# Kernel tuning notes

Hardware: AMD Instinct MI355X
Metric: run time of the kernel (lower is better)

The kernel has to match this reference:

```python
import jax, jax.numpy as jnp
import numpy as np

# dims
B, T = 2, 256            # batch, seq_len
V, H_CP, R = 512, 2, 2   # vocab, CP horizon, CP rank
E, L, NH, NPOS = 768, 12, 12, 1024  # n_embd, n_layer, n_head, max positions
HD = E // NH             # head dim = 64


def _ln(x, g, b, eps=1e-5):
    m = jnp.mean(x, -1, keepdims=True)
    v = jnp.mean((x - m) ** 2, -1, keepdims=True)
    return (x - m) * jax.lax.rsqrt(v + eps) * g + b


def setup_inputs() -> dict:
    key = jax.random.key(0)
    ks = jax.random.split(key, 10)
    s = 0.02  # GPT2 init std
    n = lambda k, sh: s * jax.random.normal(k, sh, jnp.float32)
    return {
        "input_ids": jax.random.randint(ks[0], (B, T), 0, V, dtype=jnp.int32),
        "wte": n(ks[1], (V, E)),
        "wpe": n(ks[2], (NPOS, E)),
        "ln1_g": jnp.ones((L, E), jnp.float32), "ln1_b": jnp.zeros((L, E), jnp.float32),
        "ln2_g": jnp.ones((L, E), jnp.float32), "ln2_b": jnp.zeros((L, E), jnp.float32),
        "w_qkv": n(ks[3], (L, E, 3 * E)), "b_qkv": jnp.zeros((L, 3 * E), jnp.float32),
        "w_ao": n(ks[4], (L, E, E)), "b_ao": jnp.zeros((L, E), jnp.float32),
        "w_fc": n(ks[5], (L, E, 4 * E)), "b_fc": jnp.zeros((L, 4 * E), jnp.float32),
        "w_mo": n(ks[6], (L, 4 * E, E)), "b_mo": jnp.zeros((L, E), jnp.float32),
        "lnf_g": jnp.ones((E,), jnp.float32), "lnf_b": jnp.zeros((E,), jnp.float32),
        "w_cp": n(ks[7], (E, H_CP * V * R)), "b_cp": jnp.zeros((H_CP * V * R,), jnp.float32),
    }


def reference(input_ids, wte, wpe, ln1_g, ln1_b, ln2_g, ln2_b, w_qkv, b_qkv,
              w_ao, b_ao, w_fc, b_fc, w_mo, b_mo, lnf_g, lnf_b, w_cp, b_cp):
    # --- GPT2 transformer body (eval mode: dropout inactive) ---
    h = wte[input_ids] + wpe[:T]                      # (B,T,E)
    causal = jnp.tril(jnp.ones((T, T), bool))
    inv_sqrt_hd = float(1.0 / np.sqrt(HD))

    def block(h, p):
        l1g, l1b, l2g, l2b, wq, bq, wa, ba, wf, bf, wm, bm = p
        x = _ln(h, l1g, l1b)
        qkv = x @ wq + bq                             # (B,T,3E)
        q, k, v = jnp.split(qkv, 3, axis=-1)
        q = q.reshape(B, T, NH, HD).transpose(0, 2, 1, 3)
        k = k.reshape(B, T, NH, HD).transpose(0, 2, 1, 3)
        v = v.reshape(B, T, NH, HD).transpose(0, 2, 1, 3)
        att = jnp.einsum('bhqd,bhkd->bhqk', q, k) * inv_sqrt_hd
        att = jnp.where(causal, att, jnp.float32(-1e9))
        att = jax.nn.softmax(att, axis=-1)
        o = jnp.einsum('bhqk,bhkd->bhqd', att, v).transpose(0, 2, 1, 3).reshape(B, T, E)
        h = h + o @ wa + ba
        x = _ln(h, l2g, l2b)
        h = h + jax.nn.gelu(x @ wf + bf, approximate=True) @ wm + bm  # gelu_new
        return h, None

    h, _ = jax.lax.scan(block, h, (ln1_g, ln1_b, ln2_g, ln2_b, w_qkv, b_qkv,
                                   w_ao, b_ao, w_fc, b_fc, w_mo, b_mo))
    h = _ln(h, lnf_g, lnf_b)                          # last_hidden_state

    # --- CP joint distribution: sum_r outer(f0_r, f1_r), then positivity(exp) ---
    cp = (h.reshape(B * T, E) @ w_cp + b_cp).reshape(B * T, H_CP, V, R)
    scores = jnp.einsum('nir,njr->nij', cp[:, 0], cp[:, 1])  # (B*T, V, V)
    mjd = jnp.exp(scores).reshape(B, T, V, V)[:, :-H_CP].reshape(-1, V, V)

    # --- windowed targets: targets[b,t,h] = input_ids[b, t+1+h] ---
    off = jnp.arange(T - H_CP)[:, None] + 1 + jnp.arange(H_CP)[None, :]
    tgt = input_ids[:, off].reshape(-1, H_CP)         # (B*(T-H), H)

    # --- entropy loss over unnormalized joint: mean(log Z - log p_target) ---
    n = mjd.shape[0]
    p_t = mjd[jnp.arange(n), tgt[:, 0], tgt[:, 1]]
    Z = mjd.sum((1, 2))
    loss = jnp.mean(jnp.log(Z) - jnp.log(p_t))
    return loss
```

## Files before the change

### kernel.cpp

```cpp
#include <hip/hip_runtime.h>

typedef unsigned short u16;
typedef short short8 __attribute__((ext_vector_type(8)));
typedef float f32x4 __attribute__((ext_vector_type(4)));

constexpr int B_  = 2;
constexpr int T_  = 256;
constexpr int V_  = 512;
constexpr int E_  = 768;
constexpr int L_  = 12;
constexpr int NH_ = 12;
constexpr int HD_ = 64;
constexpr int E3_ = 3 * E_;
constexpr int E4_ = 4 * E_;
constexpr int CPD_ = 2048;
constexpr int NTOK_ = B_ * T_;
constexpr int NVALID_ = B_ * (T_ - 2);
constexpr size_t PS_ = (size_t)NTOK_ * E_;
constexpr size_t QS_ = (size_t)NTOK_ * E3_;
constexpr size_t FS_ = (size_t)NTOK_ * E4_;
constexpr size_t CS_ = (size_t)NTOK_ * CPD_;

__device__ __forceinline__ u16 f2b(float f) {
    union { float f; unsigned int u; } c; c.f = f;
    unsigned int r = (c.u + 0x7FFFu + ((c.u >> 16) & 1u)) >> 16; return (u16)r;
}

__global__ __launch_bounds__(256) void embed_k(const int* __restrict__ ids,
    const float* __restrict__ wte, const float* __restrict__ wpe,
    float* __restrict__ h) {
    int n = blockIdx.x;
    int t = n % T_;
    int tok = ids[n];
    for (int e = threadIdx.x; e < E_; e += 256)
        h[n * E_ + e] = wte[tok * E_ + e] + wpe[t * E_ + e];
}

__global__ __launch_bounds__(256) void ln_res_k(float* __restrict__ h,
    const float* __restrict__ pb, int np,
    const float* __restrict__ g, const float* __restrict__ bta,
    u16* __restrict__ out) {
    int n = blockIdx.x;
    int tid = threadIdx.x;
    size_t off = (size_t)n * E_;
    float v0 = h[off + tid], v1 = h[off + tid + 256], v2 = h[off + tid + 512];
    for (int j = 0; j < np; j++) {
        const float* p = pb + (size_t)j * PS_ + off;
        v0 += p[tid]; v1 += p[tid + 256]; v2 += p[tid + 512];
    }
    if (np) { h[off + tid] = v0; h[off + tid + 256] = v1; h[off + tid + 512] = v2; }
    __shared__ float red[256];
    red[tid] = v0 + v1 + v2;
    __syncthreads();
    for (int o = 128; o > 0; o >>= 1) { if (tid < o) red[tid] += red[tid + o]; __syncthreads(); }
    float mean = red[0] * (1.0f / E_);
    __syncthreads();
    float d0 = v0 - mean, d1 = v1 - mean, d2 = v2 - mean;
    red[tid] = d0 * d0 + d1 * d1 + d2 * d2;
    __syncthreads();
    for (int o = 128; o > 0; o >>= 1) { if (tid < o) red[tid] += red[tid + o]; __syncthreads(); }
    float rstd = rsqrtf(red[0] * (1.0f / E_) + 1e-5f);
    u16* y = out + off;
    y[tid]       = f2b(d0 * rstd * g[tid]       + bta[tid]);
    y[tid + 256] = f2b(d1 * rstd * g[tid + 256] + bta[tid + 256]);
    y[tid + 512] = f2b(d2 * rstd * g[tid + 512] + bta[tid + 512]);
}

__global__ __launch_bounds__(512) void mgemm_k(const u16* __restrict__ A,
    const float* __restrict__ W, const float* __restrict__ bias,
    float* __restrict__ outP, int K, int KC, int N) {
    __shared__ u16 As[128 * 40];
    __shared__ u16 Bs[128 * 40];
    int tid = threadIdx.x, lane = tid & 63, wid = tid >> 6;
    int ln15 = lane & 15, quad = lane >> 4;
    int col0 = blockIdx.x * 128, row0 = blockIdx.y * 128;
    int kz = blockIdx.z, kbase = kz * KC;
    int ar = tid >> 2, ak = (tid & 3) * 8;
    const u16* Ag = A + (size_t)(row0 + ar) * K + kbase + ak;
    u16* Aw = &As[ar * 40 + ak];
    int bc = tid & 127, kg = (tid >> 7) * 8;
    const float* Wg = W + (size_t)(kbase + kg) * N + col0 + bc;
    u16* Bw = &Bs[bc * 40 + kg];
    int wr = (wid & 3) * 32, wc = (wid >> 2) * 64;

    f32x4 acc[2][4];
#pragma unroll
    for (int mt = 0; mt < 2; mt++)
#pragma unroll
        for (int nt = 0; nt < 4; nt++) acc[mt][nt] = (f32x4){0.f, 0.f, 0.f, 0.f};

    uint4 av = *(const uint4*)Ag;
    float w[8];
#pragma unroll
    for (int i = 0; i < 8; i++) w[i] = Wg[(size_t)i * N];

    for (int k0 = 0; k0 < KC; k0 += 32) {
        uint4 avn = av;
        float wn[8];
#pragma unroll
        for (int i = 0; i < 8; i++) wn[i] = w[i];
        if (k0 + 32 < KC) {
            avn = *(const uint4*)(Ag + k0 + 32);
#pragma unroll
            for (int i = 0; i < 8; i++) wn[i] = Wg[(size_t)(k0 + 32 + i) * N];
        }
        uint4 bv;
        asm("v_cvt_pk_bf16_f32 %0, %1, %2" : "=v"(bv.x) : "v"(w[0]), "v"(w[1]));
        asm("v_cvt_pk_bf16_f32 %0, %1, %2" : "=v"(bv.y) : "v"(w[2]), "v"(w[3]));
        asm("v_cvt_pk_bf16_f32 %0, %1, %2" : "=v"(bv.z) : "v"(w[4]), "v"(w[5]));
        asm("v_cvt_pk_bf16_f32 %0, %1, %2" : "=v"(bv.w) : "v"(w[6]), "v"(w[7]));
        __syncthreads();
        *(uint4*)Aw = av;
        *(uint4*)Bw = bv;
        __syncthreads();
        short8 af[2], bf[4];
#pragma unroll
        for (int mt = 0; mt < 2; mt++)
            af[mt] = *(const short8*)&As[(wr + mt * 16 + ln15) * 40 + quad * 8];
#pragma unroll
        for (int nt = 0; nt < 4; nt++)
            bf[nt] = *(const short8*)&Bs[(wc + nt * 16 + ln15) * 40 + quad * 8];
#pragma unroll
        for (int mt = 0; mt < 2; mt++)
#pragma unroll
            for (int nt = 0; nt < 4; nt++)
                acc[mt][nt] = __builtin_amdgcn_mfma_f32_16x16x32_bf16(
                    af[mt], bf[nt], acc[mt][nt], 0, 0, 0);
        av = avn;
#pragma unroll
        for (int i = 0; i < 8; i++) w[i] = wn[i];
    }
    float* dst = outP + (size_t)kz * NTOK_ * N;
#pragma unroll
    for (int mt = 0; mt < 2; mt++) {
#pragma unroll
        for (int nt = 0; nt < 4; nt++) {
            int c = col0 + wc + nt * 16 + ln15;
            float bb = (kz == 0) ? bias[c] : 0.f;
#pragma unroll
            for (int r = 0; r < 4; r++) {
                int rw = row0 + wr + mt * 16 + quad * 4 + r;
                dst[(size_t)rw * N + c] = acc[mt][nt][r] + bb;
            }
        }
    }
}

__global__ __launch_bounds__(256) void gelu_k(const float* __restrict__ p0,
    const float* __restrict__ p1, u16* __restrict__ out) {
    size_t i = ((size_t)blockIdx.x * 256 + threadIdx.x) * 4;
    float4 a = *(const float4*)&p0[i];
    float4 b = *(const float4*)&p1[i];
    float u[4] = {a.x + b.x, a.y + b.y, a.z + b.z, a.w + b.w};
    ushort4 o;
    u16* op = (u16*)&o;
#pragma unroll
    for (int j = 0; j < 4; j++) {
        float uu = u[j];
        float inner = 0.7978845608028654f * (uu + 0.044715f * uu * uu * uu);
        op[j] = f2b(0.5f * uu * (1.0f + tanhf(inner)));
    }
    *(ushort4*)&out[i] = o;
}

constexpr int KSTR_ = 72;
constexpr int PSTR_ = 264;
__global__ __launch_bounds__(256) void fattn_k(const float* __restrict__ qp,
    u16* __restrict__ o) {
    __shared__ u16 Ks[256 * KSTR_];
    __shared__ u16 Vt[64 * PSTR_];
    __shared__ u16 Ps[64 * PSTR_];
    int qt = blockIdx.x;
    int bh = blockIdx.y;
    int hh = bh % NH_, b = bh / NH_;
    int tid = threadIdx.x, lane = tid & 63, wid = tid >> 6;
    int ln15 = lane & 15, quad = lane >> 4;

    int sr = tid >> 4, sd = (tid & 15) * 4;
#pragma unroll
    for (int pass = 0; pass < 16; pass++) {
        int rr = sr + pass * 16;
        size_t rowbase = (size_t)(b * T_ + rr) * E3_ + hh * HD_ + sd;
        float kx = 0.f, ky = 0.f, kz = 0.f, kw = 0.f;
        float vx = 0.f, vy = 0.f, vz = 0.f, vw = 0.f;
#pragma unroll
        for (int pi = 0; pi < 4; pi++) {
            float4 kk = *(const float4*)&qp[pi * QS_ + rowbase + E_];
            float4 vv = *(const float4*)&qp[pi * QS_ + rowbase + 2 * E_];
            kx += kk.x; ky += kk.y; kz += kk.z; kw += kk.w;
            vx += vv.x; vy += vv.y; vz += vv.z; vw += vv.w;
        }
        uint2 pk;
        asm("v_cvt_pk_bf16_f32 %0, %1, %2" : "=v"(pk.x) : "v"(kx), "v"(ky));
        asm("v_cvt_pk_bf16_f32 %0, %1, %2" : "=v"(pk.y) : "v"(kz), "v"(kw));
        *(uint2*)&Ks[rr * KSTR_ + sd] = pk;
        Vt[(sd + 0) * PSTR_ + rr] = f2b(vx);
        Vt[(sd + 1) * PSTR_ + rr] = f2b(vy);
        Vt[(sd + 2) * PSTR_ + rr] = f2b(vz);
        Vt[(sd + 3) * PSTR_ + rr] = f2b(vw);
    }

    size_t qbase = (size_t)(b * T_ + qt * 64 + wid * 16 + ln15) * E3_ + hh * HD_;
    short8 qf[2];
#pragma unroll
    for (int ks = 0; ks < 2; ks++) {
        float s8[8] = {0.f, 0.f, 0.f, 0.f, 0.f, 0.f, 0.f, 0.f};
#pragma unroll
        for (int pi = 0; pi < 4; pi++) {
            const float* src = &qp[pi * QS_ + qbase + ks * 32 + quad * 8];
            float4 a = *(const float4*)src;
            float4 b4 = *(const float4*)(src + 4);
            s8[0] += a.x; s8[1] += a.y; s8[2] += a.z; s8[3] += a.w;
            s8[4] += b4.x; s8[5] += b4.y; s8[6] += b4.z; s8[7] += b4.w;
        }
        union { short8 s; unsigned int u[4]; } uq;
#pragma unroll
        for (int i = 0; i < 4; i++)
            asm("v_cvt_pk_bf16_f32 %0, %1, %2" : "=v"(uq.u[i]) : "v"(s8[2 * i]), "v"(s8[2 * i + 1]));
        qf[ks] = uq.s;
    }

    __syncthreads();

    f32x4 s[16];
#pragma unroll
    for (int nt = 0; nt < 16; nt++) s[nt] = (f32x4){0.f, 0.f, 0.f, 0.f};
#pragma unroll
    for (int ks = 0; ks < 2; ks++) {
#pragma unroll
        for (int nt = 0; nt < 16; nt++) {
            short8 kf = *(const short8*)&Ks[(nt * 16 + ln15) * KSTR_ + ks * 32 + quad * 8];
            s[nt] = __builtin_amdgcn_mfma_f32_16x16x32_bf16(qf[ks], kf, s[nt], 0, 0, 0);
        }
    }

#pragma unroll
    for (int r = 0; r < 4; r++) {
        int q = qt * 64 + wid * 16 + quad * 4 + r;
        float m = -1e30f;
#pragma unroll
        for (int nt = 0; nt < 16; nt++) {
            int j = nt * 16 + ln15;
            float sv = (j <= q) ? s[nt][r] * 0.125f : -1e9f;
            s[nt][r] = sv;
            m = fmaxf(m, sv);
        }
        m = fmaxf(m, __shfl_xor(m, 1));
        m = fmaxf(m, __shfl_xor(m, 2));
        m = fmaxf(m, __shfl_xor(m, 4));
        m = fmaxf(m, __shfl_xor(m, 8));
        float sum = 0.f;
#pragma unroll
        for (int nt = 0; nt < 16; nt++) {
            float p = __expf(s[nt][r] - m);
            s[nt][r] = p;
            sum += p;
        }
        sum += __shfl_xor(sum, 1);
        sum += __shfl_xor(sum, 2);
        sum += __shfl_xor(sum, 4);
        sum += __shfl_xor(sum, 8);
        float inv = 1.0f / sum;
#pragma unroll
        for (int nt = 0; nt < 16; nt++) s[nt][r] *= inv;
    }

#pragma unroll
    for (int nt = 0; nt < 16; nt++)
#pragma unroll
        for (int r = 0; r < 4; r++)
            Ps[(wid * 16 + quad * 4 + r) * PSTR_ + nt * 16 + ln15] = f2b(s[nt][r]);

    __syncthreads();

    f32x4 oacc[4];
#pragma unroll
    for (int dt = 0; dt < 4; dt++) oacc[dt] = (f32x4){0.f, 0.f, 0.f, 0.f};
#pragma unroll
    for (int ks = 0; ks < 8; ks++) {
        short8 pf = *(const short8*)&Ps[(wid * 16 + ln15) * PSTR_ + ks * 32 + quad * 8];
#pragma unroll
        for (int dt = 0; dt < 4; dt++) {
            short8 vf = *(const short8*)&Vt[(dt * 16 + ln15) * PSTR_ + ks * 32 + quad * 8];
            oacc[dt] = __builtin_amdgcn_mfma_f32_16x16x32_bf16(pf, vf, oacc[dt], 0, 0, 0);
        }
    }

#pragma unroll
    for (int dt = 0; dt < 4; dt++) {
#pragma unroll
        for (int r = 0; r < 4; r++) {
            int q = qt * 64 + wid * 16 + quad * 4 + r;
            o[(size_t)(b * T_ + q) * E_ + hh * HD_ + dt * 16 + ln15] = f2b(oacc[dt][r]);
        }
    }
}

__global__ __launch_bounds__(256) void zloss_k(const float* __restrict__ cp,
    const int* __restrict__ ids, float* __restrict__ lossv) {
    int n = blockIdx.x;
    int b = n / (T_ - 2), t = n % (T_ - 2);
    int nf = b * T_ + t;
    size_t base = (size_t)nf * CPD_;
    __shared__ float A0[V_], A1[V_], B0[V_], B1[V_];
    __shared__ float red[256];
    int tid = threadIdx.x;
    for (int v = tid; v < V_; v += 256) {
        float a0 = 0.f, a1 = 0.f, b0 = 0.f, b1 = 0.f;
#pragma unroll
        for (int pi = 0; pi < 4; pi++) {
            const float* ap = cp + pi * CS_ + base;
            float2 av = *(const float2*)&ap[2 * v];
            float2 bv = *(const float2*)&ap[1024 + 2 * v];
            a0 += av.x; a1 += av.y; b0 += bv.x; b1 += bv.y;
        }
        A0[v] = a0; A1[v] = a1; B0[v] = b0; B1[v] = b1;
    }
    __syncthreads();
    float acc = 0.f;
    for (int j = tid; j < V_; j += 256) {
        float b0 = B0[j], b1 = B1[j];
        for (int i = 0; i < V_; i++)
            acc += __expf(A0[i] * b0 + A1[i] * b1);
    }
    red[tid] = acc; __syncthreads();
    for (int off = 128; off > 0; off >>= 1) { if (tid < off) red[tid] += red[tid + off]; __syncthreads(); }
    if (tid == 0) {
        int t0 = ids[b * T_ + t + 1];
        int t1 = ids[b * T_ + t + 2];
        float score = A0[t0] * B0[t1] + A1[t0] * B1[t1];
        lossv[n] = logf(red[0]) - score;
    }
}

__global__ __launch_bounds__(256) void reduce_k(const float* __restrict__ lossv,
    unsigned int* __restrict__ out) {
    __shared__ float red[256];
    int tid = threadIdx.x;
    float s = 0.f;
    for (int i = tid; i < NVALID_; i += 256) s += lossv[i];
    red[tid] = s; __syncthreads();
    for (int off = 128; off > 0; off >>= 1) { if (tid < off) red[tid] += red[tid + off]; __syncthreads(); }
    if (tid == 0) {
        float loss = red[0] / (float)NVALID_;
        union { float f; unsigned int u; } cv; cv.f = loss;
        unsigned int b = (cv.u + 0x7FFFu + ((cv.u >> 16) & 1u)) >> 16;
        out[0] = (b << 16) | b;
    }
}

extern "C" void kernel_launch(void* const* d_in, const int* in_sizes, int n_in,
                              void* d_out, int out_size, void* d_ws, size_t ws_size,
                              hipStream_t stream) {
    const int*   ids  = (const int*)d_in[0];
    const float* wte  = (const float*)d_in[1];
    const float* wpe  = (const float*)d_in[2];
    const float* ln1g = (const float*)d_in[3];
    const float* ln1b = (const float*)d_in[4];
    const float* ln2g = (const float*)d_in[5];
    const float* ln2b = (const float*)d_in[6];
    const float* wqkv = (const float*)d_in[7];
    const float* bqkv = (const float*)d_in[8];
    const float* wao  = (const float*)d_in[9];
    const float* bao  = (const float*)d_in[10];
    const float* wfc  = (const float*)d_in[11];
    const float* bfc  = (const float*)d_in[12];
    const float* wmo  = (const float*)d_in[13];
    const float* bmo  = (const float*)d_in[14];
    const float* lnfg = (const float*)d_in[15];
    const float* lnfb = (const float*)d_in[16];
    const float* wcp  = (const float*)d_in[17];
    const float* bcp  = (const float*)d_in[18];

    char* p = (char*)d_ws;
    float* h    = (float*)p; p += (size_t)NTOK_ * E_ * 4;
    u16*   x    = (u16*)p;   p += (size_t)NTOK_ * E_ * 2;
    u16*   aob  = (u16*)p;   p += (size_t)NTOK_ * E_ * 2;
    u16*   fcb  = (u16*)p;   p += (size_t)NTOK_ * E4_ * 2;
    float* pbuf = (float*)p; p += 4 * QS_ * 4;
    float* lossv = (float*)p; p += 4096;

    embed_k<<<NTOK_, 256, 0, stream>>>(ids, wte, wpe, h);
    for (int l = 0; l < L_; l++) {
        ln_res_k<<<NTOK_, 256, 0, stream>>>(h, pbuf, l ? 8 : 0,
                                            ln1g + l * E_, ln1b + l * E_, x);
        mgemm_k<<<dim3(E3_ / 128, 4, 4), 512, 0, stream>>>(
            x, wqkv + (size_t)l * E_ * E3_, bqkv + l * E3_, pbuf, E_, 192, E3_);
        fattn_k<<<dim3(4, B_ * NH_), 256, 0, stream>>>(pbuf, aob);
        mgemm_k<<<dim3(E_ / 128, 4, 8), 512, 0, stream>>>(
            aob, wao + (size_t)l * E_ * E_, bao + l * E_, pbuf, E_, 96, E_);
        ln_res_k<<<NTOK_, 256, 0, stream>>>(h, pbuf, 8,
                                            ln2g + l * E_, ln2b + l * E_, x);
        mgemm_k<<<dim3(E4_ / 128, 4, 2), 512, 0, stream>>>(
            x, wfc + (size_t)l * E_ * E4_, bfc + l * E4_, pbuf, E_, 384, E4_);
        gelu_k<<<(NTOK_ * E4_) / 1024, 256, 0, stream>>>(pbuf, pbuf + FS_, fcb);
        mgemm_k<<<dim3(E_ / 128, 4, 8), 512, 0, stream>>>(
            fcb, wmo + (size_t)l * E4_ * E_, bmo + l * E_, pbuf, E4_, 384, E_);
    }
    ln_res_k<<<NTOK_, 256, 0, stream>>>(h, pbuf, 8, lnfg, lnfb, x);
    mgemm_k<<<dim3(CPD_ / 128, 4, 4), 512, 0, stream>>>(
        x, wcp, bcp, pbuf, E_, 192, CPD_);
    zloss_k<<<NVALID_, 256, 0, stream>>>(pbuf, ids, lossv);
    reduce_k<<<1, 256, 0, stream>>>(lossv, (unsigned int*)d_out);
}
```

Baseline: 1.324 ms.

## Use 256-row GEMM tiles with templated column width and rebalance split-K

The GEMM kernel becomes a template with 256-row tiles and either 128- or 64-column tiles, so each block reuses every converted weight tile across twice as many rows. This cuts the redundant global fp32 weight loads and bf16 conversions that came from having four row blocks. Split-K factors are raised for the QKV, FC and CP projections, and the consumers (attention, GELU, zloss) now sum 6, 4 or 8 partial buffers. The cost is a larger partial-sum workspace, more partial-sum traffic in the consumer kernels, and more accumulator registers per thread.

```diff
diff --git a/kernel.cpp b/kernel.cpp
--- a/kernel.cpp
+++ b/kernel.cpp
@@ -66,73 +66,92 @@
     y[tid + 512] = f2b(d2 * rstd * g[tid + 512] + bta[tid + 512]);
 }
 
+template<int BN>
 __global__ __launch_bounds__(512) void mgemm_k(const u16* __restrict__ A,
     const float* __restrict__ W, const float* __restrict__ bias,
     float* __restrict__ outP, int K, int KC, int N) {
-    __shared__ u16 As[128 * 40];
-    __shared__ u16 Bs[128 * 40];
+    __shared__ u16 As[256 * 40];
+    __shared__ u16 Bs[BN * 40];
+    constexpr int MT = (BN == 128) ? 4 : 2;
+    constexpr int NW = (BN == 128) ? 8 : 4;
     int tid = threadIdx.x, lane = tid & 63, wid = tid >> 6;
     int ln15 = lane & 15, quad = lane >> 4;
-    int col0 = blockIdx.x * 128, row0 = blockIdx.y * 128;
+    int col0 = blockIdx.x * BN, row0 = blockIdx.y * 256;
     int kz = blockIdx.z, kbase = kz * KC;
     int ar = tid >> 2, ak = (tid & 3) * 8;
-    const u16* Ag = A + (size_t)(row0 + ar) * K + kbase + ak;
-    u16* Aw = &As[ar * 40 + ak];
-    int bc = tid & 127, kg = (tid >> 7) * 8;
+    const u16* Ag0 = A + (size_t)(row0 + ar) * K + kbase + ak;
+    const u16* Ag1 = Ag0 + (size_t)128 * K;
+    u16* Aw0 = &As[ar * 40 + ak];
+    u16* Aw1 = &As[(ar + 128) * 40 + ak];
+    int wr, wc, bc, kg;
+    if constexpr (BN == 128) {
+        wr = (wid & 3) * 64; wc = (wid >> 2) * 64;
+        bc = tid & 127; kg = (tid >> 7) * 8;
+    } else {
+        wr = wid * 32; wc = 0;
+        bc = tid & 63; kg = (tid >> 6) * 4;
+    }
     const float* Wg = W + (size_t)(kbase + kg) * N + col0 + bc;
     u16* Bw = &Bs[bc * 40 + kg];
-    int wr = (wid & 3) * 32, wc = (wid >> 2) * 64;
-
-    f32x4 acc[2][4];
-#pragma unroll
-    for (int mt = 0; mt < 2; mt++)
+
+    f32x4 acc[MT][4];
+#pragma unroll
+    for (int mt = 0; mt < MT; mt++)
 #pragma unroll
         for (int nt = 0; nt < 4; nt++) acc[mt][nt] = (f32x4){0.f, 0.f, 0.f, 0.f};
 
-    uint4 av = *(const uint4*)Ag;
-    float w[8];
-#pragma unroll
-    for (int i = 0; i < 8; i++) w[i] = Wg[(size_t)i * N];
+    uint4 av0 = *(const uint4*)Ag0;
+    uint4 av1 = *(const uint4*)Ag1;
+    float w[NW];
+#pragma unroll
+    for (int i = 0; i < NW; i++) w[i] = Wg[(size_t)i * N];
 
     for (int k0 = 0; k0 < KC; k0 += 32) {
-        uint4 avn = av;
-        float wn[8];
-#pragma unroll
-        for (int i = 0; i < 8; i++) wn[i] = w[i];
+        uint4 an0 = av0, an1 = av1;
+        float wn[NW];
+#pragma unroll
+        for (int i = 0; i < NW; i++) wn[i] = w[i];
         if (k0 + 32 < KC) {
-            avn = *(const uint4*)(Ag + k0 + 32);
-#pragma unroll
-            for (int i = 0; i < 8; i++) wn[i] = Wg[(size_t)(k0 + 32 + i) * N];
-        }
-        uint4 bv;
-        asm("v_cvt_pk_bf16_f32 %0, %1, %2" : "=v"(bv.x) : "v"(w[0]), "v"(w[1]));
-        asm("v_cvt_pk_bf16_f32 %0, %1, %2" : "=v"(bv.y) : "v"(w[2]), "v"(w[3]));
-        asm("v_cvt_pk_bf16_f32 %0, %1, %2" : "=v"(bv.z) : "v"(w[4]), "v"(w[5]));
-        asm("v_cvt_pk_bf16_f32 %0, %1, %2" : "=v"(bv.w) : "v"(w[6]), "v"(w[7]));
+            an0 = *(const uint4*)(Ag0 + k0 + 32);
+            an1 = *(const uint4*)(Ag1 + k0 + 32);
+#pragma unroll
+            for (int i = 0; i < NW; i++) wn[i] = Wg[(size_t)(k0 + 32 + i) * N];
+        }
+        unsigned int bvw[NW / 2];
+#pragma unroll
+        for (int i = 0; i < NW / 2; i++)
+            asm("v_cvt_pk_bf16_f32 %0, %1, %2" : "=v"(bvw[i]) : "v"(w[2 * i]), "v"(w[2 * i + 1]));
         __syncthreads();
-        *(uint4*)Aw = av;
-        *(uint4*)Bw = bv;
+        *(uint4*)Aw0 = av0;
+        *(uint4*)Aw1 = av1;
+        if constexpr (BN == 128) {
+            uint4 bv; bv.x = bvw[0]; bv.y = bvw[1]; bv.z = bvw[2]; bv.w = bvw[3];
+            *(uint4*)Bw = bv;
+        } else {
+            uint2 bv; bv.x = bvw[0]; bv.y = bvw[1];
+            *(uint2*)Bw = bv;
+        }
         __syncthreads();
-        short8 af[2], bf[4];
-#pragma unroll
-        for (int mt = 0; mt < 2; mt++)
+        short8 af[MT], bf[4];
+#pragma unroll
+        for (int mt = 0; mt < MT; mt++)
             af[mt] = *(const short8*)&As[(wr + mt * 16 + ln15) * 40 + quad * 8];
 #pragma unroll
         for (int nt = 0; nt < 4; nt++)
             bf[nt] = *(const short8*)&Bs[(wc + nt * 16 + ln15) * 40 + quad * 8];
 #pragma unroll
-        for (int mt = 0; mt < 2; mt++)
+        for (int mt = 0; mt < MT; mt++)
 #pragma unroll
             for (int nt = 0; nt < 4; nt++)
                 acc[mt][nt] = __builtin_amdgcn_mfma_f32_16x16x32_bf16(
                     af[mt], bf[nt], acc[mt][nt], 0, 0, 0);
-        av = avn;
-#pragma unroll
-        for (int i = 0; i < 8; i++) w[i] = wn[i];
+        av0 = an0; av1 = an1;
+#pragma unroll
+        for (int i = 0; i < NW; i++) w[i] = wn[i];
     }
     float* dst = outP + (size_t)kz * NTOK_ * N;
 #pragma unroll
-    for (int mt = 0; mt < 2; mt++) {
+    for (int mt = 0; mt < MT; mt++) {
 #pragma unroll
         for (int nt = 0; nt < 4; nt++) {
             int c = col0 + wc + nt * 16 + ln15;
@@ -146,12 +165,16 @@
     }
 }
 
-__global__ __launch_bounds__(256) void gelu_k(const float* __restrict__ p0,
-    const float* __restrict__ p1, u16* __restrict__ out) {
+__global__ __launch_bounds__(256) void gelu_k(const float* __restrict__ pb,
+    u16* __restrict__ out) {
     size_t i = ((size_t)blockIdx.x * 256 + threadIdx.x) * 4;
-    float4 a = *(const float4*)&p0[i];
-    float4 b = *(const float4*)&p1[i];
-    float u[4] = {a.x + b.x, a.y + b.y, a.z + b.z, a.w + b.w};
+    float4 a = *(const float4*)&pb[i];
+    float u[4] = {a.x, a.y, a.z, a.w};
+#pragma unroll
+    for (int j = 1; j < 4; j++) {
+        float4 b = *(const float4*)&pb[(size_t)j * FS_ + i];
+        u[0] += b.x; u[1] += b.y; u[2] += b.z; u[3] += b.w;
+    }
     ushort4 o;
     u16* op = (u16*)&o;
 #pragma unroll
@@ -184,7 +207,7 @@
         float kx = 0.f, ky = 0.f, kz = 0.f, kw = 0.f;
         float vx = 0.f, vy = 0.f, vz = 0.f, vw = 0.f;
 #pragma unroll
-        for (int pi = 0; pi < 4; pi++) {
+        for (int pi = 0; pi < 6; pi++) {
             float4 kk = *(const float4*)&qp[pi * QS_ + rowbase + E_];
             float4 vv = *(const float4*)&qp[pi * QS_ + rowbase + 2 * E_];
             kx += kk.x; ky += kk.y; kz += kk.z; kw += kk.w;
@@ -206,7 +229,7 @@
     for (int ks = 0; ks < 2; ks++) {
         float s8[8] = {0.f, 0.f, 0.f, 0.f, 0.f, 0.f, 0.f, 0.f};
 #pragma unroll
-        for (int pi = 0; pi < 4; pi++) {
+        for (int pi = 0; pi < 6; pi++) {
             const float* src = &qp[pi * QS_ + qbase + ks * 32 + quad * 8];
             float4 a = *(const float4*)src;
             float4 b4 = *(const float4*)(src + 4);
@@ -308,7 +331,7 @@
     for (int v = tid; v < V_; v += 256) {
         float a0 = 0.f, a1 = 0.f, b0 = 0.f, b1 = 0.f;
 #pragma unroll
-        for (int pi = 0; pi < 4; pi++) {
+        for (int pi = 0; pi < 8; pi++) {
             const float* ap = cp + pi * CS_ + base;
             float2 av = *(const float2*)&ap[2 * v];
             float2 bv = *(const float2*)&ap[1024 + 2 * v];
@@ -377,29 +400,29 @@
     u16*   x    = (u16*)p;   p += (size_t)NTOK_ * E_ * 2;
     u16*   aob  = (u16*)p;   p += (size_t)NTOK_ * E_ * 2;
     u16*   fcb  = (u16*)p;   p += (size_t)NTOK_ * E4_ * 2;
-    float* pbuf = (float*)p; p += 4 * QS_ * 4;
+    float* pbuf = (float*)p; p += 8 * CS_ * 4;
     float* lossv = (float*)p; p += 4096;
 
     embed_k<<<NTOK_, 256, 0, stream>>>(ids, wte, wpe, h);
     for (int l = 0; l < L_; l++) {
         ln_res_k<<<NTOK_, 256, 0, stream>>>(h, pbuf, l ? 8 : 0,
                                             ln1g + l * E_, ln1b + l * E_, x);
-        mgemm_k<<<dim3(E3_ / 128, 4, 4), 512, 0, stream>>>(
-            x, wqkv + (size_t)l * E_ * E3_, bqkv + l * E3_, pbuf, E_, 192, E3_);
+        mgemm_k<128><<<dim3(E3_ / 128, 2, 6), 512, 0, stream>>>(
+            x, wqkv + (size_t)l * E_ * E3_, bqkv + l * E3_, pbuf, E_, 128, E3_);
         fattn_k<<<dim3(4, B_ * NH_), 256, 0, stream>>>(pbuf, aob);
-        mgemm_k<<<dim3(E_ / 128, 4, 8), 512, 0, stream>>>(
+        mgemm_k<64><<<dim3(E_ / 64, 2, 8), 512, 0, stream>>>(
             aob, wao + (size_t)l * E_ * E_, bao + l * E_, pbuf, E_, 96, E_);
         ln_res_k<<<NTOK_, 256, 0, stream>>>(h, pbuf, 8,
                                             ln2g + l * E_, ln2b + l * E_, x);
-        mgemm_k<<<dim3(E4_ / 128, 4, 2), 512, 0, stream>>>(
-            x, wfc + (size_t)l * E_ * E4_, bfc + l * E4_, pbuf, E_, 384, E4_);
-        gelu_k<<<(NTOK_ * E4_) / 1024, 256, 0, stream>>>(pbuf, pbuf + FS_, fcb);
-        mgemm_k<<<dim3(E_ / 128, 4, 8), 512, 0, stream>>>(
+        mgemm_k<128><<<dim3(E4_ / 128, 2, 4), 512, 0, stream>>>(
+            x, wfc + (size_t)l * E_ * E4_, bfc + l * E4_, pbuf, E_, 192, E4_);
+        gelu_k<<<(NTOK_ * E4_) / 1024, 256, 0, stream>>>(pbuf, fcb);
+        mgemm_k<64><<<dim3(E_ / 64, 2, 8), 512, 0, stream>>>(
             fcb, wmo + (size_t)l * E4_ * E_, bmo + l * E_, pbuf, E4_, 384, E_);
     }
     ln_res_k<<<NTOK_, 256, 0, stream>>>(h, pbuf, 8, lnfg, lnfb, x);
-    mgemm_k<<<dim3(CPD_ / 128, 4, 4), 512, 0, stream>>>(
-        x, wcp, bcp, pbuf, E_, 192, CPD_);
+    mgemm_k<128><<<dim3(CPD_ / 128, 2, 8), 512, 0, stream>>>(
+        x, wcp, bcp, pbuf, E_, 96, CPD_);
     zloss_k<<<NVALID_, 256, 0, stream>>>(pbuf, ids, lossv);
     reduce_k<<<1, 256, 0, stream>>>(lossv, (unsigned int*)d_out);
 }
```

Result: slower. 1.377 ms (+4.0%).

## Retile GEMM to full-M 512x64 blocks and fuse embedding into first layernorm

Applied to the files above, without the earlier changes.

The GEMM kernel now computes all 512 token rows per block with a 64-column tile, so each fp32 weight element is loaded and converted to bf16 once instead of once per 128-row block. This reduces weight traffic, the main memory cost at this small M. In exchange, the grid has fewer blocks and each wave holds more accumulators. The embedding gather is also folded into the first layernorm launch via a negative np flag, removing a separate kernel.

```diff
diff --git a/kernel.cpp b/kernel.cpp
--- a/kernel.cpp
+++ b/kernel.cpp
@@ -26,29 +26,32 @@
     unsigned int r = (c.u + 0x7FFFu + ((c.u >> 16) & 1u)) >> 16; return (u16)r;
 }
 
-__global__ __launch_bounds__(256) void embed_k(const int* __restrict__ ids,
-    const float* __restrict__ wte, const float* __restrict__ wpe,
-    float* __restrict__ h) {
-    int n = blockIdx.x;
-    int t = n % T_;
-    int tok = ids[n];
-    for (int e = threadIdx.x; e < E_; e += 256)
-        h[n * E_ + e] = wte[tok * E_ + e] + wpe[t * E_ + e];
-}
-
 __global__ __launch_bounds__(256) void ln_res_k(float* __restrict__ h,
     const float* __restrict__ pb, int np,
+    const int* __restrict__ ids, const float* __restrict__ wte,
+    const float* __restrict__ wpe,
     const float* __restrict__ g, const float* __restrict__ bta,
     u16* __restrict__ out) {
     int n = blockIdx.x;
     int tid = threadIdx.x;
     size_t off = (size_t)n * E_;
-    float v0 = h[off + tid], v1 = h[off + tid + 256], v2 = h[off + tid + 512];
-    for (int j = 0; j < np; j++) {
-        const float* p = pb + (size_t)j * PS_ + off;
-        v0 += p[tid]; v1 += p[tid + 256]; v2 += p[tid + 512];
-    }
-    if (np) { h[off + tid] = v0; h[off + tid + 256] = v1; h[off + tid + 512] = v2; }
+    float v0, v1, v2;
+    if (np < 0) {
+        int t = n % T_;
+        int tok = ids[n];
+        size_t wo = (size_t)tok * E_, po = (size_t)t * E_;
+        v0 = wte[wo + tid]       + wpe[po + tid];
+        v1 = wte[wo + tid + 256] + wpe[po + tid + 256];
+        v2 = wte[wo + tid + 512] + wpe[po + tid + 512];
+        h[off + tid] = v0; h[off + tid + 256] = v1; h[off + tid + 512] = v2;
+    } else {
+        v0 = h[off + tid]; v1 = h[off + tid + 256]; v2 = h[off + tid + 512];
+        for (int j = 0; j < np; j++) {
+            const float* p = pb + (size_t)j * PS_ + off;
+            v0 += p[tid]; v1 += p[tid + 256]; v2 += p[tid + 512];
+        }
+        if (np) { h[off + tid] = v0; h[off + tid + 256] = v1; h[off + tid + 512] = v2; }
+    }
     __shared__ float red[256];
     red[tid] = v0 + v1 + v2;
     __syncthreads();
@@ -69,88 +72,93 @@
 __global__ __launch_bounds__(512) void mgemm_k(const u16* __restrict__ A,
     const float* __restrict__ W, const float* __restrict__ bias,
     float* __restrict__ outP, int K, int KC, int N) {
-    __shared__ u16 As[128 * 40];
-    __shared__ u16 Bs[128 * 40];
+    __shared__ u16 As[512 * 40];
+    __shared__ u16 Bs[64 * 40];
     int tid = threadIdx.x, lane = tid & 63, wid = tid >> 6;
     int ln15 = lane & 15, quad = lane >> 4;
-    int col0 = blockIdx.x * 128, row0 = blockIdx.y * 128;
-    int kz = blockIdx.z, kbase = kz * KC;
+    int col0 = blockIdx.x * 64;
+    int kz = blockIdx.y, kbase = kz * KC;
     int ar = tid >> 2, ak = (tid & 3) * 8;
-    const u16* Ag = A + (size_t)(row0 + ar) * K + kbase + ak;
+    const u16* Ag = A + (size_t)ar * K + kbase + ak;
     u16* Aw = &As[ar * 40 + ak];
-    int bc = tid & 127, kg = (tid >> 7) * 8;
+    int bc = tid & 63, kg = (tid >> 6) * 4;
     const float* Wg = W + (size_t)(kbase + kg) * N + col0 + bc;
     u16* Bw = &Bs[bc * 40 + kg];
-    int wr = (wid & 3) * 32, wc = (wid >> 2) * 64;
-
-    f32x4 acc[2][4];
-#pragma unroll
-    for (int mt = 0; mt < 2; mt++)
+    int wr = wid * 64;
+
+    f32x4 acc[4][4];
+#pragma unroll
+    for (int mt = 0; mt < 4; mt++)
 #pragma unroll
         for (int nt = 0; nt < 4; nt++) acc[mt][nt] = (f32x4){0.f, 0.f, 0.f, 0.f};
 
-    uint4 av = *(const uint4*)Ag;
-    float w[8];
-#pragma unroll
-    for (int i = 0; i < 8; i++) w[i] = Wg[(size_t)i * N];
+    uint4 av[4];
+#pragma unroll
+    for (int j = 0; j < 4; j++) av[j] = *(const uint4*)(Ag + (size_t)j * 128 * K);
+    float w[4];
+#pragma unroll
+    for (int i = 0; i < 4; i++) w[i] = Wg[(size_t)i * N];
 
     for (int k0 = 0; k0 < KC; k0 += 32) {
-        uint4 avn = av;
-        float wn[8];
-#pragma unroll
-        for (int i = 0; i < 8; i++) wn[i] = w[i];
+        uint4 an[4]; float wn[4];
+#pragma unroll
+        for (int j = 0; j < 4; j++) an[j] = av[j];
+#pragma unroll
+        for (int i = 0; i < 4; i++) wn[i] = w[i];
         if (k0 + 32 < KC) {
-            avn = *(const uint4*)(Ag + k0 + 32);
-#pragma unroll
-            for (int i = 0; i < 8; i++) wn[i] = Wg[(size_t)(k0 + 32 + i) * N];
-        }
-        uint4 bv;
+#pragma unroll
+            for (int j = 0; j < 4; j++)
+                an[j] = *(const uint4*)(Ag + (size_t)j * 128 * K + k0 + 32);
+#pragma unroll
+            for (int i = 0; i < 4; i++) wn[i] = Wg[(size_t)(k0 + 32 + i) * N];
+        }
+        uint2 bv;
         asm("v_cvt_pk_bf16_f32 %0, %1, %2" : "=v"(bv.x) : "v"(w[0]), "v"(w[1]));
         asm("v_cvt_pk_bf16_f32 %0, %1, %2" : "=v"(bv.y) : "v"(w[2]), "v"(w[3]));
-        asm("v_cvt_pk_bf16_f32 %0, %1, %2" : "=v"(bv.z) : "v"(w[4]), "v"(w[5]));
-        asm("v_cvt_pk_bf16_f32 %0, %1, %2" : "=v"(bv.w) : "v"(w[6]), "v"(w[7]));
         __syncthreads();
-        *(uint4*)Aw = av;
-        *(uint4*)Bw = bv;
+#pragma unroll
+        for (int j = 0; j < 4; j++) *(uint4*)(Aw + j * 128 * 40) = av[j];
+        *(uint2*)Bw = bv;
         __syncthreads();
-        short8 af[2], bf[4];
-#pragma unroll
-        for (int mt = 0; mt < 2; mt++)
+        short8 af[4], bf[4];
+#pragma unroll
+        for (int mt = 0; mt < 4; mt++)
             af[mt] = *(const short8*)&As[(wr + mt * 16 + ln15) * 40 + quad * 8];
 #pragma unroll
         for (int nt = 0; nt < 4; nt++)
-            bf[nt] = *(const short8*)&Bs[(wc + nt * 16 + ln15) * 40 + quad * 8];
-#pragma unroll
-        for (int mt = 0; mt < 2; mt++)
+            bf[nt] = *(const short8*)&Bs[(nt * 16 + ln15) * 40 + quad * 8];
+#pragma unroll
+        for (int mt = 0; mt < 4; mt++)
 #pragma unroll
             for (int nt = 0; nt < 4; nt++)
                 acc[mt][nt] = __builtin_amdgcn_mfma_f32_16x16x32_bf16(
                     af[mt], bf[nt], acc[mt][nt], 0, 0, 0);
-        av = avn;
-#pragma unroll
-        for (int i = 0; i < 8; i++) w[i] = wn[i];
+#pragma unroll
+        for (int j = 0; j < 4; j++) av[j] = an[j];
+#pragma unroll
+        for (int i = 0; i < 4; i++) w[i] = wn[i];
     }
     float* dst = outP + (size_t)kz * NTOK_ * N;
 #pragma unroll
-    for (int mt = 0; mt < 2; mt++) {
+    for (int mt = 0; mt < 4; mt++) {
 #pragma unroll
         for (int nt = 0; nt < 4; nt++) {
-            int c = col0 + wc + nt * 16 + ln15;
+            int c = col0 + nt * 16 + ln15;
             float bb = (kz == 0) ? bias[c] : 0.f;
 #pragma unroll
             for (int r = 0; r < 4; r++) {
-                int rw = row0 + wr + mt * 16 + quad * 4 + r;
+                int rw = wr + mt * 16 + quad * 4 + r;
                 dst[(size_t)rw * N + c] = acc[mt][nt][r] + bb;
             }
         }
     }
 }
 
-__global__ __launch_bounds__(256) void gelu_k(const float* __restrict__ p0,
-    const float* __restrict__ p1, u16* __restrict__ out) {
+__global__ __launch_bounds__(256) void gelu_k(const float* __restrict__ pb,
+    u16* __restrict__ out) {
     size_t i = ((size_t)blockIdx.x * 256 + threadIdx.x) * 4;
-    float4 a = *(const float4*)&p0[i];
-    float4 b = *(const float4*)&p1[i];
+    float4 a = *(const float4*)&pb[i];
+    float4 b = *(const float4*)&pb[FS_ + i];
     float u[4] = {a.x + b.x, a.y + b.y, a.z + b.z, a.w + b.w};
     ushort4 o;
     u16* op = (u16*)&o;
@@ -380,25 +388,24 @@
     float* pbuf = (float*)p; p += 4 * QS_ * 4;
     float* lossv = (float*)p; p += 4096;
 
-    embed_k<<<NTOK_, 256, 0, stream>>>(ids, wte, wpe, h);
     for (int l = 0; l < L_; l++) {
-        ln_res_k<<<NTOK_, 256, 0, stream>>>(h, pbuf, l ? 8 : 0,
+        ln_res_k<<<NTOK_, 256, 0, stream>>>(h, pbuf, l ? 8 : -1, ids, wte, wpe,
                                             ln1g + l * E_, ln1b + l * E_, x);
-        mgemm_k<<<dim3(E3_ / 128, 4, 4), 512, 0, stream>>>(
+        mgemm_k<<<dim3(E3_ / 64, 4), 512, 0, stream>>>(
             x, wqkv + (size_t)l * E_ * E3_, bqkv + l * E3_, pbuf, E_, 192, E3_);
         fattn_k<<<dim3(4, B_ * NH_), 256, 0, stream>>>(pbuf, aob);
-        mgemm_k<<<dim3(E_ / 128, 4, 8), 512, 0, stream>>>(
+        mgemm_k<<<dim3(E_ / 64, 8), 512, 0, stream>>>(
             aob, wao + (size_t)l * E_ * E_, bao + l * E_, pbuf, E_, 96, E_);
-        ln_res_k<<<NTOK_, 256, 0, stream>>>(h, pbuf, 8,
+        ln_res_k<<<NTOK_, 256, 0, stream>>>(h, pbuf, 8, ids, wte, wpe,
                                             ln2g + l * E_, ln2b + l * E_, x);
-        mgemm_k<<<dim3(E4_ / 128, 4, 2), 512, 0, stream>>>(
+        mgemm_k<<<dim3(E4_ / 64, 2), 512, 0, stream>>>(
             x, wfc + (size_t)l * E_ * E4_, bfc + l * E4_, pbuf, E_, 384, E4_);
-        gelu_k<<<(NTOK_ * E4_) / 1024, 256, 0, stream>>>(pbuf, pbuf + FS_, fcb);
-        mgemm_k<<<dim3(E_ / 128, 4, 8), 512, 0, stream>>>(
+        gelu_k<<<(NTOK_ * E4_) / 1024, 256, 0, stream>>>(pbuf, fcb);
+        mgemm_k<<<dim3(E_ / 64, 8), 512, 0, stream>>>(
             fcb, wmo + (size_t)l * E4_ * E_, bmo + l * E_, pbuf, E4_, 384, E_);
     }
-    ln_res_k<<<NTOK_, 256, 0, stream>>>(h, pbuf, 8, lnfg, lnfb, x);
-    mgemm_k<<<dim3(CPD_ / 128, 4, 4), 512, 0, stream>>>(
+    ln_res_k<<<NTOK_, 256, 0, stream>>>(h, pbuf, 8, ids, wte, wpe, lnfg, lnfb, x);
+    mgemm_k<<<dim3(CPD_ / 64, 4), 512, 0, stream>>>(
         x, wcp, bcp, pbuf, E_, 192, CPD_);
     zloss_k<<<NVALID_, 256, 0, stream>>>(pbuf, ids, lossv);
     reduce_k<<<1, 256, 0, stream>>>(lossv, (unsigned int*)d_out);
```

Measured after the change: 3.548 ms. 168% more time.
